# Optimization experiments

Measured on AMD Instinct MI355X. Metric: run time of the kernel, lower is better.

Reference implementation:

```python
import jax, jax.numpy as jnp
import numpy as np

B, S, D = 4, 4096, 128

def setup_inputs() -> dict:
    key = jax.random.key(0)
    kq, kk, kv = jax.random.split(key, 3)
    q = jax.random.normal(kq, (B, S, D), dtype=jnp.float32)
    k = jax.random.normal(kk, (B, S, D), dtype=jnp.float32)
    v = jax.random.normal(kv, (B, S, D), dtype=jnp.float32)
    return {"q": q, "k": k, "v": v}

def reference(q, k, v):
    d_model = q.shape[-1]
    scale = 1.0 / jnp.sqrt(jnp.asarray(d_model, q.dtype))
    # [B, S, S] scores
    scores = jnp.einsum('bqd,bkd->bqk', q, k) * scale
    s = q.shape[1]
    causal = jnp.tril(jnp.ones((s, s), dtype=bool))
    neg_inf = jnp.asarray(-jnp.inf, scores.dtype)
    scores = jnp.where(causal[None, :, :], scores, neg_inf)
    attn = jax.nn.softmax(scores, axis=-1)
    return jnp.einsum('bqk,bkd->bqd', attn, v)
```

## Files before the change

kernel.cpp:

```cpp
#include <hip/hip_runtime.h>


#define B_   4
#define S_   4096
#define D_   128
#define BN   64
#define NT_  64
#define QT_  32
#define RMAX 4
#define BLOB_SHORTS 16384
#define MASKVAL (-1.0e30f)

typedef __attribute__((ext_vector_type(8))) short bf16x8;
typedef __attribute__((ext_vector_type(4))) float f32x4;
typedef __attribute__((ext_vector_type(16))) float f32x16;

__device__ __forceinline__ short f2bf(float x) {
    unsigned u = __builtin_bit_cast(unsigned, x);
    unsigned r = (u + 0x7fffu + ((u >> 16) & 1u)) >> 16;
    return (short)r;
}
__device__ __forceinline__ float ex2(float x) { return __builtin_amdgcn_exp2f(x); }
__device__ __forceinline__ unsigned pkbf(float lo, float hi) {
    return (unsigned)(unsigned short)f2bf(lo) | ((unsigned)(unsigned short)f2bf(hi) << 16);
}
__device__ __forceinline__ void gl_lds16(const short* g, short* l) {
    __builtin_amdgcn_global_load_lds(
        (const __attribute__((address_space(1))) unsigned int*)g,
        (__attribute__((address_space(3))) unsigned int*)l, 16, 0, 0);
}

__global__ __launch_bounds__(256) void prep(const float* __restrict__ Qg,
                                            const float* __restrict__ Kg,
                                            const float* __restrict__ Vg,
                                            short* __restrict__ Qbf,
                                            short* __restrict__ KV)
{
    __shared__ short vt[64][40];
    const int id  = blockIdx.x;
    const int tid = threadIdx.x;
    const float SC = 0.12751740f;

    if (id < 1024) {
        const int b = id & 3, tile = (id >> 2) & 63, q4 = id >> 8;
        const int n = q4 * 16 + (tid >> 4);
        const int G = tid & 15;
        const size_t rowoff = ((size_t)b * S_ + (size_t)tile * 64 + n) * D_ + G * 8;
        short* blob = KV + (size_t)(b * NT_ + tile) * BLOB_SHORTS;
        {
            float4 a = *reinterpret_cast<const float4*>(Qg + rowoff);
            float4 c = *reinterpret_cast<const float4*>(Qg + rowoff + 4);
            bf16x8 v;
            v[0] = f2bf(a.x * SC); v[1] = f2bf(a.y * SC); v[2] = f2bf(a.z * SC); v[3] = f2bf(a.w * SC);
            v[4] = f2bf(c.x * SC); v[5] = f2bf(c.y * SC); v[6] = f2bf(c.z * SC); v[7] = f2bf(c.w * SC);
            *reinterpret_cast<bf16x8*>(Qbf + rowoff) = v;
        }
        {
            float4 a = *reinterpret_cast<const float4*>(Kg + rowoff);
            float4 c = *reinterpret_cast<const float4*>(Kg + rowoff + 4);
            bf16x8 v;
            v[0] = f2bf(a.x); v[1] = f2bf(a.y); v[2] = f2bf(a.z); v[3] = f2bf(a.w);
            v[4] = f2bf(c.x); v[5] = f2bf(c.y); v[6] = f2bf(c.z); v[7] = f2bf(c.w);
            const int p = (G & 8) | ((G & 7) ^ (n & 7));
            *reinterpret_cast<bf16x8*>(blob + n * 128 + p * 8) = v;
        }
    } else {
        const int u = id - 1024;
        const int b = u & 3, tile = (u >> 2) & 63, dq = u >> 8;
        short* blob = KV + (size_t)(b * NT_ + tile) * BLOB_SHORTS;
        {
            const int n = tid >> 2, c8 = tid & 3;
            const size_t off = ((size_t)b * S_ + (size_t)tile * 64 + n) * D_ + dq * 32 + c8 * 8;
            float4 a = *reinterpret_cast<const float4*>(Vg + off);
            float4 c = *reinterpret_cast<const float4*>(Vg + off + 4);
            bf16x8 v;
            v[0] = f2bf(a.x); v[1] = f2bf(a.y); v[2] = f2bf(a.z); v[3] = f2bf(a.w);
            v[4] = f2bf(c.x); v[5] = f2bf(c.y); v[6] = f2bf(c.z); v[7] = f2bf(c.w);
            *reinterpret_cast<bf16x8*>(&vt[n][c8 * 8]) = v;
        }
        __syncthreads();
        {
            const int dl = tid >> 3, G = tid & 7;
            const int d  = dq * 32 + dl;
            bf16x8 g;
#pragma unroll
            for (int i = 0; i < 8; ++i) g[i] = vt[G * 8 + i][dl];
            const int p = G ^ (d & 7);
            *reinterpret_cast<bf16x8*>(blob + 8192 + d * 64 + p * 8) = g;
        }
    }
}

template<bool SPLIT>
__global__ __launch_bounds__(256, 2) void fa_fwd(const short* __restrict__ Qbf,
                                                 const short* __restrict__ KV,
                                                 float* __restrict__ Og,
                                                 float* __restrict__ Op,
                                                 float* __restrict__ Ml,
                                                 int R)
{
    __shared__ short lkv[2][BLOB_SHORTS];

    const int tid  = threadIdx.x;
    const int wv   = tid >> 6;
    const int lane = tid & 63;
    const int col  = lane & 31;
    const int half = lane >> 5;
    const int c7   = col & 7;

    int batch, t, lo, hi, chunk_id;
    {
        const int id = blockIdx.x;
        batch = id & 3;
        if (SPLIT) {
            int u = id >> 2;
            int tt = u / R;
            int r  = u - tt * R;
            t  = QT_ - 1 - tt;
            const int nk = 2 * t + 2;
            lo = r * nk / R;
            hi = (r + 1) * nk / R;
            chunk_id = (batch * QT_ + t) * R + r;
            if (lo >= hi) return;
        } else {
            t  = QT_ - 1 - (id >> 2);
            lo = 0; hi = 2 * t + 2; chunk_id = 0;
        }
    }

    bf16x8 qf[8];
    {
        const short* qp = Qbf + ((size_t)batch * S_ + (size_t)t * 128 + wv * 32 + col) * D_ + half * 8;
#pragma unroll
        for (int c = 0; c < 8; ++c)
            qf[c] = *reinterpret_cast<const bf16x8*>(qp + c * 16);
    }

    f32x16 acc[4];
#pragma unroll
    for (int i = 0; i < 4; ++i)
#pragma unroll
        for (int r = 0; r < 16; ++r) acc[i][r] = 0.f;
    float mrun = MASKVAL, lrun = 0.f;

    const size_t tilebase = (size_t)batch * NT_ * BLOB_SHORTS;
#define STAGE(KT, BUF) do {                                                   \
        const short* g_ = KV + tilebase + (size_t)(KT) * BLOB_SHORTS + tid * 8;\
        short* l_ = (BUF) + tid * 8;                                          \
        _Pragma("unroll")                                                     \
        for (int c_ = 0; c_ < 8; ++c_)                                        \
            gl_lds16(g_ + c_ * 2048, l_ + c_ * 2048);                         \
    } while (0)

    STAGE(lo, lkv[0]);

    for (int kt = lo; kt < hi; ++kt) {
        const short* cur = lkv[(kt - lo) & 1];
        short* nxt = lkv[(kt - lo + 1) & 1];
        __syncthreads();
        if (kt + 1 < hi) STAGE(kt + 1, nxt);

        const short* lk = cur;
        const short* lv = cur + 8192;

        f32x16 st[2];
#pragma unroll
        for (int i = 0; i < 2; ++i)
#pragma unroll
            for (int r = 0; r < 16; ++r) st[i][r] = 0.f;
#pragma unroll
        for (int c = 0; c < 8; ++c) {
            const int G = 2 * c + half;
            const int p = (G & 8) | ((G & 7) ^ c7);
#pragma unroll
            for (int kt32 = 0; kt32 < 2; ++kt32) {
                const int n = kt32 * 32 + col;
                bf16x8 kf = *reinterpret_cast<const bf16x8*>(lk + n * 128 + p * 8);
                st[kt32] = __builtin_amdgcn_mfma_f32_32x32x16_bf16(kf, qf[c], st[kt32], 0, 0, 0);
            }
        }

        if (kt >= 2 * t) {
            const int kbase = (kt - 2 * t) * 64;
            const int qloc  = wv * 32 + col;
#pragma unroll
            for (int kt32 = 0; kt32 < 2; ++kt32)
#pragma unroll
                for (int r = 0; r < 16; ++r) {
                    const int kl = kt32 * 32 + (r & 3) + 8 * (r >> 2) + 4 * half;
                    if (kbase + kl > qloc) st[kt32][r] = MASKVAL;
                }
        }

        float mx = MASKVAL;
#pragma unroll
        for (int i = 0; i < 2; ++i)
#pragma unroll
            for (int r = 0; r < 16; ++r) mx = fmaxf(mx, st[i][r]);
        mx = fmaxf(mx, __shfl_xor(mx, 32));
        const float mnew = fmaxf(mrun, mx);
        const float al   = ex2(mrun - mnew);
        mrun = mnew;
        float sum = 0.f;
#pragma unroll
        for (int i = 0; i < 2; ++i)
#pragma unroll
            for (int r = 0; r < 16; ++r) {
                float pv = ex2(st[i][r] - mnew);
                st[i][r] = pv;
                sum += pv;
            }
        sum += __shfl_xor(sum, 32);
        lrun = lrun * al + sum;
#pragma unroll
        for (int i = 0; i < 4; ++i)
#pragma unroll
            for (int r = 0; r < 16; ++r) acc[i][r] *= al;

#pragma unroll
        for (int kt32 = 0; kt32 < 2; ++kt32) {
            unsigned pw[4][2];
#pragma unroll
            for (int w = 0; w < 4; ++w) {
                pw[w][0] = pkbf(st[kt32][4 * w],     st[kt32][4 * w + 1]);
                pw[w][1] = pkbf(st[kt32][4 * w + 2], st[kt32][4 * w + 3]);
            }
#pragma unroll
            for (int s1 = 0; s1 < 2; ++s1) {
                unsigned snd0 = pw[2 * s1 + 1 - half][0];
                unsigned snd1 = pw[2 * s1 + 1 - half][1];
                unsigned rcv0 = __shfl_xor((int)snd0, 32);
                unsigned rcv1 = __shfl_xor((int)snd1, 32);
                unsigned own0 = pw[2 * s1 + half][0];
                unsigned own1 = pw[2 * s1 + half][1];
                int4 wi;
                wi.x = (int)(half ? rcv0 : own0);
                wi.y = (int)(half ? rcv1 : own1);
                wi.z = (int)(half ? own0 : rcv0);
                wi.w = (int)(half ? own1 : rcv1);
                bf16x8 pf = __builtin_bit_cast(bf16x8, wi);
                const int step = kt32 * 2 + s1;
                const int G = 2 * step + half;
                const int p = G ^ c7;
#pragma unroll
                for (int dt = 0; dt < 4; ++dt) {
                    const int d = dt * 32 + col;
                    bf16x8 vf = *reinterpret_cast<const bf16x8*>(lv + d * 64 + p * 8);
                    acc[dt] = __builtin_amdgcn_mfma_f32_32x32x16_bf16(vf, pf, acc[dt], 0, 0, 0);
                }
            }
        }
    }
#undef STAGE

    const int qloc = wv * 32 + col;
    if (SPLIT) {
        float* ob = Op + (size_t)chunk_id * (128 * D_) + (size_t)qloc * D_;
#pragma unroll
        for (int dt = 0; dt < 4; ++dt)
#pragma unroll
            for (int g = 0; g < 4; ++g) {
                const int d0 = dt * 32 + 8 * g + 4 * half;
                f32x4 v4 = {acc[dt][4 * g], acc[dt][4 * g + 1], acc[dt][4 * g + 2], acc[dt][4 * g + 3]};
                *reinterpret_cast<f32x4*>(ob + d0) = v4;
            }
        if (half == 0) {
            float* mlb = Ml + (size_t)chunk_id * (128 * 2) + qloc * 2;
            mlb[0] = mrun;
            mlb[1] = lrun;
        }
    } else {
        const float inv = 1.0f / lrun;
        float* og = Og + ((size_t)batch * S_ + (size_t)t * 128 + qloc) * D_;
#pragma unroll
        for (int dt = 0; dt < 4; ++dt)
#pragma unroll
            for (int g = 0; g < 4; ++g) {
                const int d0 = dt * 32 + 8 * g + 4 * half;
                f32x4 v4 = {acc[dt][4 * g] * inv, acc[dt][4 * g + 1] * inv,
                            acc[dt][4 * g + 2] * inv, acc[dt][4 * g + 3] * inv};
                *reinterpret_cast<f32x4*>(og + d0) = v4;
            }
    }
}

template<int RR>
__global__ __launch_bounds__(256) void fa_merge(const float* __restrict__ Op,
                                                const float* __restrict__ Ml,
                                                float* __restrict__ Og)
{
    const int x   = blockIdx.x;
    const int btq = x >> 4;
    const int oct = x & 15;
    const int t   = btq & (QT_ - 1);
    const int nk  = 2 * t + 2;
    const int row = oct * 8 + (threadIdx.x >> 5);
    const int cg  = threadIdx.x & 31;
    const size_t cbase = (size_t)btq * RR;

    float mg = MASKVAL;
#pragma unroll
    for (int r = 0; r < RR; ++r) {
        int lo = r * nk / RR, hi = (r + 1) * nk / RR;
        if (lo < hi) mg = fmaxf(mg, Ml[(cbase + r) * (128 * 2) + row * 2]);
    }
    float l = 0.f;
    f32x4 a = (f32x4){0.f, 0.f, 0.f, 0.f};
#pragma unroll
    for (int r = 0; r < RR; ++r) {
        int lo = r * nk / RR, hi = (r + 1) * nk / RR;
        if (lo >= hi) continue;
        float mr = Ml[(cbase + r) * (128 * 2) + row * 2];
        float lr = Ml[(cbase + r) * (128 * 2) + row * 2 + 1];
        float w  = ex2(mr - mg);
        l += lr * w;
        a += w * *reinterpret_cast<const f32x4*>(Op + (cbase + r) * (128 * D_) + row * D_ + cg * 4);
    }
    *reinterpret_cast<f32x4*>(Og + (size_t)btq * (128 * D_) + row * D_ + cg * 4) = a * (1.0f / l);
}

extern "C" void kernel_launch(void* const* d_in, const int* in_sizes, int n_in,
                              void* d_out, int out_size, void* d_ws, size_t ws_size,
                              hipStream_t stream) {
    const float* q = (const float*)d_in[0];
    const float* k = (const float*)d_in[1];
    const float* v = (const float*)d_in[2];
    float* o = (float*)d_out;

    const size_t QBF_BYTES = (size_t)B_ * S_ * D_ * 2;
    const size_t KV_BYTES  = (size_t)B_ * NT_ * BLOB_SHORTS * 2;
    const size_t PREFIX    = QBF_BYTES + KV_BYTES;
    const size_t O_FLOATS  = (size_t)B_ * QT_ * 128 * D_;
    const size_t ML_FLOATS = (size_t)B_ * QT_ * 128 * 2;
    const size_t PER_R     = (O_FLOATS + ML_FLOATS) * sizeof(float);

    char* ws = (char*)d_ws;
    short* Qbf = (short*)ws;
    short* KV  = (short*)(ws + QBF_BYTES);

    int R = 0;
    if (ws_size > PREFIX) {
        R = (int)((ws_size - PREFIX) / PER_R);
        if (R > RMAX) R = RMAX;
    }

    prep<<<dim3(2048), 256, 0, stream>>>(q, k, v, Qbf, KV);

    if (R >= 1) {
        float* Op = (float*)(ws + PREFIX);
        float* Ml = Op + (size_t)R * O_FLOATS;
        fa_fwd<true><<<dim3(B_ * QT_ * R), 256, 0, stream>>>(Qbf, KV, nullptr, Op, Ml, R);
        switch (R) {
            case 1: fa_merge<1><<<dim3(B_ * QT_ * 16), 256, 0, stream>>>(Op, Ml, o); break;
            case 2: fa_merge<2><<<dim3(B_ * QT_ * 16), 256, 0, stream>>>(Op, Ml, o); break;
            case 3: fa_merge<3><<<dim3(B_ * QT_ * 16), 256, 0, stream>>>(Op, Ml, o); break;
            default: fa_merge<4><<<dim3(B_ * QT_ * 16), 256, 0, stream>>>(Op, Ml, o); break;
        }
    } else {
        fa_fwd<false><<<dim3(B_ * QT_), 256, 0, stream>>>(Qbf, KV, o, nullptr, nullptr, 1);
    }
}
```

Measured before the change: 124.9 us.

## Single-buffer LDS for higher occupancy, fuse Q conversion, bf16 partials

Moves the Q fp32-to-bf16 conversion and scaling from the prep kernel into the attention kernel, which drops the Qbf workspace round trip. The K/V LDS double buffer becomes a single buffer with a sync before and after each tile load, and launch bounds rise from 2 to 4 blocks per CU to hide latency through occupancy instead of prefetch. Split partial outputs are stored as bf16 rather than fp32 to halve partial-output traffic in the merge. Risks: global-to-LDS loads are no longer overlapped with MFMA work within a block, the extra syncs add stalls, register pressure at 4 blocks/CU may cause spills, and bf16 partials lose precision.

```diff
diff --git a/kernel.cpp b/kernel.cpp
--- a/kernel.cpp
+++ b/kernel.cpp
@@ -4,7 +4,6 @@
 #define B_   4
 #define S_   4096
 #define D_   128
-#define BN   64
 #define NT_  64
 #define QT_  32
 #define RMAX 4
@@ -24,22 +23,22 @@
 __device__ __forceinline__ unsigned pkbf(float lo, float hi) {
     return (unsigned)(unsigned short)f2bf(lo) | ((unsigned)(unsigned short)f2bf(hi) << 16);
 }
+__device__ __forceinline__ float bf2f(short s) {
+    return __builtin_bit_cast(float, ((unsigned)(unsigned short)s) << 16);
+}
 __device__ __forceinline__ void gl_lds16(const short* g, short* l) {
     __builtin_amdgcn_global_load_lds(
         (const __attribute__((address_space(1))) unsigned int*)g,
         (__attribute__((address_space(3))) unsigned int*)l, 16, 0, 0);
 }
 
-__global__ __launch_bounds__(256) void prep(const float* __restrict__ Qg,
-                                            const float* __restrict__ Kg,
+__global__ __launch_bounds__(256) void prep(const float* __restrict__ Kg,
                                             const float* __restrict__ Vg,
-                                            short* __restrict__ Qbf,
                                             short* __restrict__ KV)
 {
     __shared__ short vt[64][40];
     const int id  = blockIdx.x;
     const int tid = threadIdx.x;
-    const float SC = 0.12751740f;
 
     if (id < 1024) {
         const int b = id & 3, tile = (id >> 2) & 63, q4 = id >> 8;
@@ -47,23 +46,13 @@
         const int G = tid & 15;
         const size_t rowoff = ((size_t)b * S_ + (size_t)tile * 64 + n) * D_ + G * 8;
         short* blob = KV + (size_t)(b * NT_ + tile) * BLOB_SHORTS;
-        {
-            float4 a = *reinterpret_cast<const float4*>(Qg + rowoff);
-            float4 c = *reinterpret_cast<const float4*>(Qg + rowoff + 4);
-            bf16x8 v;
-            v[0] = f2bf(a.x * SC); v[1] = f2bf(a.y * SC); v[2] = f2bf(a.z * SC); v[3] = f2bf(a.w * SC);
-            v[4] = f2bf(c.x * SC); v[5] = f2bf(c.y * SC); v[6] = f2bf(c.z * SC); v[7] = f2bf(c.w * SC);
-            *reinterpret_cast<bf16x8*>(Qbf + rowoff) = v;
-        }
-        {
-            float4 a = *reinterpret_cast<const float4*>(Kg + rowoff);
-            float4 c = *reinterpret_cast<const float4*>(Kg + rowoff + 4);
-            bf16x8 v;
-            v[0] = f2bf(a.x); v[1] = f2bf(a.y); v[2] = f2bf(a.z); v[3] = f2bf(a.w);
-            v[4] = f2bf(c.x); v[5] = f2bf(c.y); v[6] = f2bf(c.z); v[7] = f2bf(c.w);
-            const int p = (G & 8) | ((G & 7) ^ (n & 7));
-            *reinterpret_cast<bf16x8*>(blob + n * 128 + p * 8) = v;
-        }
+        float4 a = *reinterpret_cast<const float4*>(Kg + rowoff);
+        float4 c = *reinterpret_cast<const float4*>(Kg + rowoff + 4);
+        bf16x8 v;
+        v[0] = f2bf(a.x); v[1] = f2bf(a.y); v[2] = f2bf(a.z); v[3] = f2bf(a.w);
+        v[4] = f2bf(c.x); v[5] = f2bf(c.y); v[6] = f2bf(c.z); v[7] = f2bf(c.w);
+        const int p = (G & 8) | ((G & 7) ^ (n & 7));
+        *reinterpret_cast<bf16x8*>(blob + n * 128 + p * 8) = v;
     } else {
         const int u = id - 1024;
         const int b = u & 3, tile = (u >> 2) & 63, dq = u >> 8;
@@ -92,14 +81,14 @@
 }
 
 template<bool SPLIT>
-__global__ __launch_bounds__(256, 2) void fa_fwd(const short* __restrict__ Qbf,
+__global__ __launch_bounds__(256, 4) void fa_fwd(const float* __restrict__ Qg,
                                                  const short* __restrict__ KV,
                                                  float* __restrict__ Og,
-                                                 float* __restrict__ Op,
+                                                 short* __restrict__ Opb,
                                                  float* __restrict__ Ml,
                                                  int R)
 {
-    __shared__ short lkv[2][BLOB_SHORTS];
+    __shared__ short lkv[BLOB_SHORTS];
 
     const int tid  = threadIdx.x;
     const int wv   = tid >> 6;
@@ -130,10 +119,17 @@
 
     bf16x8 qf[8];
     {
-        const short* qp = Qbf + ((size_t)batch * S_ + (size_t)t * 128 + wv * 32 + col) * D_ + half * 8;
-#pragma unroll
-        for (int c = 0; c < 8; ++c)
-            qf[c] = *reinterpret_cast<const bf16x8*>(qp + c * 16);
+        const float SC = 0.12751740f;
+        const float* qp = Qg + ((size_t)batch * S_ + (size_t)t * 128 + wv * 32 + col) * D_ + half * 8;
+#pragma unroll
+        for (int c = 0; c < 8; ++c) {
+            float4 a = *reinterpret_cast<const float4*>(qp + c * 16);
+            float4 b = *reinterpret_cast<const float4*>(qp + c * 16 + 4);
+            bf16x8 v;
+            v[0] = f2bf(a.x * SC); v[1] = f2bf(a.y * SC); v[2] = f2bf(a.z * SC); v[3] = f2bf(a.w * SC);
+            v[4] = f2bf(b.x * SC); v[5] = f2bf(b.y * SC); v[6] = f2bf(b.z * SC); v[7] = f2bf(b.w * SC);
+            qf[c] = v;
+        }
     }
 
     f32x16 acc[4];
@@ -144,24 +140,21 @@
     float mrun = MASKVAL, lrun = 0.f;
 
     const size_t tilebase = (size_t)batch * NT_ * BLOB_SHORTS;
-#define STAGE(KT, BUF) do {                                                   \
+#define STAGE(KT) do {                                                        \
         const short* g_ = KV + tilebase + (size_t)(KT) * BLOB_SHORTS + tid * 8;\
-        short* l_ = (BUF) + tid * 8;                                          \
+        short* l_ = lkv + tid * 8;                                            \
         _Pragma("unroll")                                                     \
         for (int c_ = 0; c_ < 8; ++c_)                                        \
             gl_lds16(g_ + c_ * 2048, l_ + c_ * 2048);                         \
     } while (0)
 
-    STAGE(lo, lkv[0]);
-
     for (int kt = lo; kt < hi; ++kt) {
-        const short* cur = lkv[(kt - lo) & 1];
-        short* nxt = lkv[(kt - lo + 1) & 1];
         __syncthreads();
-        if (kt + 1 < hi) STAGE(kt + 1, nxt);
-
-        const short* lk = cur;
-        const short* lv = cur + 8192;
+        STAGE(kt);
+        __syncthreads();
+
+        const short* lk = lkv;
+        const short* lv = lkv + 8192;
 
         f32x16 st[2];
 #pragma unroll
@@ -255,14 +248,16 @@
 
     const int qloc = wv * 32 + col;
     if (SPLIT) {
-        float* ob = Op + (size_t)chunk_id * (128 * D_) + (size_t)qloc * D_;
+        short* ob = Opb + (size_t)chunk_id * (128 * D_) + (size_t)qloc * D_;
 #pragma unroll
         for (int dt = 0; dt < 4; ++dt)
 #pragma unroll
             for (int g = 0; g < 4; ++g) {
                 const int d0 = dt * 32 + 8 * g + 4 * half;
-                f32x4 v4 = {acc[dt][4 * g], acc[dt][4 * g + 1], acc[dt][4 * g + 2], acc[dt][4 * g + 3]};
-                *reinterpret_cast<f32x4*>(ob + d0) = v4;
+                int2 w;
+                w.x = (int)pkbf(acc[dt][4 * g],     acc[dt][4 * g + 1]);
+                w.y = (int)pkbf(acc[dt][4 * g + 2], acc[dt][4 * g + 3]);
+                *reinterpret_cast<int2*>(ob + d0) = w;
             }
         if (half == 0) {
             float* mlb = Ml + (size_t)chunk_id * (128 * 2) + qloc * 2;
@@ -285,7 +280,7 @@
 }
 
 template<int RR>
-__global__ __launch_bounds__(256) void fa_merge(const float* __restrict__ Op,
+__global__ __launch_bounds__(256) void fa_merge(const short* __restrict__ Opb,
                                                 const float* __restrict__ Ml,
                                                 float* __restrict__ Og)
 {
@@ -314,7 +309,12 @@
         float lr = Ml[(cbase + r) * (128 * 2) + row * 2 + 1];
         float w  = ex2(mr - mg);
         l += lr * w;
-        a += w * *reinterpret_cast<const f32x4*>(Op + (cbase + r) * (128 * D_) + row * D_ + cg * 4);
+        short4 s = *reinterpret_cast<const short4*>(
+            Opb + (cbase + r) * (128 * D_) + (size_t)row * D_ + cg * 4);
+        a[0] += w * bf2f(s.x);
+        a[1] += w * bf2f(s.y);
+        a[2] += w * bf2f(s.z);
+        a[3] += w * bf2f(s.w);
     }
     *reinterpret_cast<f32x4*>(Og + (size_t)btq * (128 * D_) + row * D_ + cg * 4) = a * (1.0f / l);
 }
@@ -327,16 +327,14 @@
     const float* v = (const float*)d_in[2];
     float* o = (float*)d_out;
 
-    const size_t QBF_BYTES = (size_t)B_ * S_ * D_ * 2;
     const size_t KV_BYTES  = (size_t)B_ * NT_ * BLOB_SHORTS * 2;
-    const size_t PREFIX    = QBF_BYTES + KV_BYTES;
-    const size_t O_FLOATS  = (size_t)B_ * QT_ * 128 * D_;
+    const size_t PREFIX    = KV_BYTES;
+    const size_t O_ELEMS   = (size_t)B_ * QT_ * 128 * D_;
     const size_t ML_FLOATS = (size_t)B_ * QT_ * 128 * 2;
-    const size_t PER_R     = (O_FLOATS + ML_FLOATS) * sizeof(float);
+    const size_t PER_R     = O_ELEMS * 2 + ML_FLOATS * 4;
 
     char* ws = (char*)d_ws;
-    short* Qbf = (short*)ws;
-    short* KV  = (short*)(ws + QBF_BYTES);
+    short* KV = (short*)ws;
 
     int R = 0;
     if (ws_size > PREFIX) {
@@ -344,19 +342,19 @@
         if (R > RMAX) R = RMAX;
     }
 
-    prep<<<dim3(2048), 256, 0, stream>>>(q, k, v, Qbf, KV);
+    prep<<<dim3(2048), 256, 0, stream>>>(k, v, KV);
 
     if (R >= 1) {
-        float* Op = (float*)(ws + PREFIX);
-        float* Ml = Op + (size_t)R * O_FLOATS;
-        fa_fwd<true><<<dim3(B_ * QT_ * R), 256, 0, stream>>>(Qbf, KV, nullptr, Op, Ml, R);
+        short* Opb = (short*)(ws + PREFIX);
+        float* Ml  = (float*)(ws + PREFIX + (size_t)R * O_ELEMS * 2);
+        fa_fwd<true><<<dim3(B_ * QT_ * R), 256, 0, stream>>>(q, KV, nullptr, Opb, Ml, R);
         switch (R) {
-            case 1: fa_merge<1><<<dim3(B_ * QT_ * 16), 256, 0, stream>>>(Op, Ml, o); break;
-            case 2: fa_merge<2><<<dim3(B_ * QT_ * 16), 256, 0, stream>>>(Op, Ml, o); break;
-            case 3: fa_merge<3><<<dim3(B_ * QT_ * 16), 256, 0, stream>>>(Op, Ml, o); break;
-            default: fa_merge<4><<<dim3(B_ * QT_ * 16), 256, 0, stream>>>(Op, Ml, o); break;
+            case 1: fa_merge<1><<<dim3(B_ * QT_ * 16), 256, 0, stream>>>(Opb, Ml, o); break;
+            case 2: fa_merge<2><<<dim3(B_ * QT_ * 16), 256, 0, stream>>>(Opb, Ml, o); break;
+            case 3: fa_merge<3><<<dim3(B_ * QT_ * 16), 256, 0, stream>>>(Opb, Ml, o); break;
+            default: fa_merge<4><<<dim3(B_ * QT_ * 16), 256, 0, stream>>>(Opb, Ml, o); break;
         }
     } else {
-        fa_fwd<false><<<dim3(B_ * QT_), 256, 0, stream>>>(Qbf, KV, o, nullptr, nullptr, 1);
-    }
-}
+        fa_fwd<false><<<dim3(B_ * QT_), 256, 0, stream>>>(q, KV, o, nullptr, nullptr, 1);
+    }
+}
```

After: 151.4 us. 21.2% more time.
